# Kernel optimization log

Measured on AMD Instinct MI355X. Metric: run time of the kernel, lower is better.

## Reference

```python
import jax, jax.numpy as jnp
import numpy as np


def l2_normalize(x, axis, eps=1e-12):
    # matches tf.nn.l2_normalize / K.l2_normalize
    return x * jax.lax.rsqrt(jnp.maximum(jnp.sum(x * x, axis=axis, keepdims=True), eps))


def setup_inputs() -> dict:
    key = jax.random.key(0)
    k1, k2 = jax.random.split(key)
    B, H, W, C = 32, 1, 900, 256
    return {
        "input_1": jax.random.normal(k1, (B, H, W, C), dtype=jnp.float32),
        "input_2": jax.random.normal(k2, (B, H, W, C), dtype=jnp.float32),
    }


def reference(input_1, input_2):
    B, H, W, C = input_1.shape
    p = W // 2
    # 'euclidean' normalization along the width (azimuth) axis, axis=2
    x1 = l2_normalize(input_1, axis=2)
    x2 = l2_normalize(input_2, axis=2)
    # RangePadding2D: circular padding along width to width 2W-1, so that a
    # VALID correlation with a W-wide kernel yields exactly W circular shifts.
    x1p = jnp.concatenate([x1[:, :, p:, :], x1, x1[:, :, : p - 1, :]], axis=2)  # [B,H,2W-1,C]
    # Per-sample correlation: out[b, j] = sum_{h,i,c} x1p[b,h,j+i,c] * x2[b,h,i,c]
    # Expressed as one grouped conv (one group per batch element) instead of tf.scan.
    lhs = jnp.transpose(x1p, (0, 3, 1, 2)).reshape(1, B * C, H, 2 * W - 1)  # NCHW
    rhs = jnp.transpose(x2, (0, 3, 1, 2))  # [B, C, H, W] OIHW
    out = jax.lax.conv_general_dilated(
        lhs, rhs,
        window_strides=(1, 1), padding="VALID",
        dimension_numbers=("NCHW", "OIHW", "NCHW"),
        feature_group_count=B,
    )  # [1, B, 1, W]
    # -> (B, H=1, W, output_dim=1), matching compute_output_shape
    return jnp.transpose(out, (1, 2, 3, 0))
```

## Files before the change

kernel.cpp:

```cpp
#include <hip/hip_runtime.h>
#include <hip/hip_bf16.h>

#define BATCH 32
#define WW 900
#define CCH 256
#define PVAL 450
#define KHALF 128
#define MSTRIP 128
#define NCHUNK 64
#define NCHUNKS 15

typedef __bf16 bf16x8 __attribute__((ext_vector_type(8)));
typedef __bf16 bf16x4 __attribute__((ext_vector_type(4)));
typedef float f32x4 __attribute__((ext_vector_type(4)));

#define INV15_OFF 245760
#define INV4_OFF  65536

__global__ void nc_norm_partial(const float* __restrict__ x1,
                                const float* __restrict__ x2,
                                float* __restrict__ sums,
                                float* __restrict__ out, int out_n,
                                int segs, int rowsper) {
    int blk = blockIdx.x;
    int oz = blk * 256 + threadIdx.x;
    if (oz < out_n) out[oz] = 0.f;
    int seg = blk % segs;
    int b = (blk / segs) & 31;
    int which = blk / (segs * 32);
    const float* x = which ? x2 : x1;
    int c = threadIdx.x;
    int r0 = seg * rowsper;
    int r1 = r0 + rowsper;
    if (r1 > WW) r1 = WW;
    const float* p = x + ((size_t)b * WW + r0) * CCH + c;
    float s = 0.f;
    #pragma unroll 4
    for (int w = 0; w < r1 - r0; ++w) {
        float v = p[(size_t)w * CCH];
        s = fmaf(v, v, s);
    }
    sums[(((size_t)(which * 32 + b)) * segs + seg) * CCH + c] = s;
}

template <int SEGS>
__global__ void nc_norm_finalize(float* __restrict__ ws, float* __restrict__ inv) {
    int i = blockIdx.x * 256 + threadIdx.x;
    int c = i & 255;
    int wb = i >> 8;
    const float* s = ws + (size_t)wb * SEGS * CCH + c;
    float t = 0.f;
    #pragma unroll
    for (int q = 0; q < SEGS; ++q) t += s[(size_t)q * CCH];
    inv[i] = rsqrtf(fmaxf(t, 1e-12f));
}

__global__ __launch_bounds__(256, 2)
void nc_corr(const float* __restrict__ x1,
             const float* __restrict__ x2,
             const float* __restrict__ invp,
             float* __restrict__ out) {
    __shared__ __bf16 Abuf[MSTRIP * KHALF];
    __shared__ __bf16 Bbuf[2][NCHUNK * KHALF];
    __shared__ float diag[2][4][96];
    __shared__ float partial[WW];

    float (*scratch)[16][97] = (float (*)[16][97])Abuf;

    const int tid = threadIdx.x;
    const int b = blockIdx.x & 31;
    const int strip = (blockIdx.x >> 5) & 7;
    const int kh = blockIdx.x >> 8;
    const int m0 = strip * MSTRIP;
    const int k0 = kh * KHALF;

    const float* __restrict__ inv1 = invp + b * CCH + k0;
    const float* __restrict__ inv2 = invp + (BATCH + b) * CCH + k0;
    const float* __restrict__ x1b = x1 + (size_t)b * WW * CCH + k0;
    const float* __restrict__ x2b = x2 + (size_t)b * WW * CCH + k0;

    const int lane = tid & 63;
    const int wave = tid >> 6;
    const int fr = lane & 15;
    const int fq = lane >> 4;

    const int sr = tid >> 5;
    const int sg = tid & 31;

    const float4 ivB = *(const float4*)(inv2 + sg * 4);
    float4 st[8];

    auto loadB = [&](int chunk) {
        #pragma unroll
        for (int k = 0; k < 8; ++k) {
            const int row = chunk * NCHUNK + sr + 8 * k;
            st[k] = (row < WW) ? *(const float4*)(x2b + (size_t)row * CCH + sg * 4)
                               : make_float4(0.f, 0.f, 0.f, 0.f);
        }
    };
    auto writeB = [&](int buf) {
        #pragma unroll
        for (int k = 0; k < 8; ++k) {
            const int row = sr + 8 * k;
            float4 f = st[k];
            bf16x4 v = { (__bf16)(f.x * ivB.x), (__bf16)(f.y * ivB.y),
                         (__bf16)(f.z * ivB.z), (__bf16)(f.w * ivB.w) };
            *(bf16x4*)(&Bbuf[buf][row * KHALF + (((sg >> 1) ^ sr) << 3) + (sg & 1) * 4]) = v;
        }
    };

    loadB(0);

    {
        float4 iv1 = *(const float4*)(inv1 + sg * 4);
        #pragma unroll
        for (int k = 0; k < 16; ++k) {
            const int row = sr + 8 * k;
            const int m = m0 + row;
            float4 f = make_float4(0.f, 0.f, 0.f, 0.f);
            if (m < WW) f = *(const float4*)(x1b + (size_t)m * CCH + sg * 4);
            bf16x4 v = { (__bf16)(f.x * iv1.x), (__bf16)(f.y * iv1.y),
                         (__bf16)(f.z * iv1.z), (__bf16)(f.w * iv1.w) };
            *(bf16x4*)(&Abuf[row * KHALF + (((sg >> 1) ^ (row & 7)) << 3) + (sg & 1) * 4]) = v;
        }
    }

    for (int i = tid; i < WW; i += 256) partial[i] = 0.f;
    writeB(0);
    __syncthreads();

    bf16x8 afm[2][4];
    #pragma unroll
    for (int mt = 0; mt < 2; ++mt)
        #pragma unroll
        for (int kk = 0; kk < 4; ++kk) {
            const int row = wave * 32 + mt * 16 + fr;
            const int g = (kk * 4 + fq) ^ (row & 7);
            afm[mt][kk] = *(const bf16x8*)(&Abuf[row * KHALF + g * 8]);
        }
    #pragma unroll
    for (int mt = 0; mt < 2; ++mt)
        #pragma unroll
        for (int kk = 0; kk < 4; ++kk)
            asm volatile("" : "+v"(afm[mt][kk]));

    __syncthreads();

    {
        float* sw = (float*)&scratch[wave][0][0];
        for (int i = lane; i < 16 * 97; i += 64) sw[i] = 0.f;
    }

    int cur = 0;
    for (int chunk = 0; chunk < NCHUNKS; ++chunk) {
        if (chunk + 1 < NCHUNKS) {
            loadB(chunk + 1);
            __builtin_amdgcn_sched_barrier(0);
        }

        f32x4 acc[2][4];
        #pragma unroll
        for (int mt = 0; mt < 2; ++mt)
            #pragma unroll
            for (int nt = 0; nt < 4; ++nt)
                acc[mt][nt] = (f32x4){0.f, 0.f, 0.f, 0.f};

        #pragma unroll
        for (int kk = 0; kk < 4; ++kk) {
            bf16x8 bfr[4];
            #pragma unroll
            for (int nt = 0; nt < 4; ++nt) {
                const int row = nt * 16 + fr;
                const int g = (kk * 4 + fq) ^ (row & 7);
                bfr[nt] = *(const bf16x8*)(&Bbuf[cur][row * KHALF + g * 8]);
            }
            #pragma unroll
            for (int mt = 0; mt < 2; ++mt)
                #pragma unroll
                for (int nt = 0; nt < 4; ++nt)
                    acc[mt][nt] = __builtin_amdgcn_mfma_f32_16x16x32_bf16(
                        afm[mt][kk], bfr[nt], acc[mt][nt], 0, 0, 0);
        }

        {
            f32x4 c0 = acc[0][3];
            f32x4 c1 = acc[0][2] + acc[1][3];
            f32x4 c2 = acc[0][1] + acc[1][2];
            f32x4 c3 = acc[0][0] + acc[1][1];
            f32x4 c4 = acc[1][0];
            const int mub = 4 * fq;
            #pragma unroll
            for (int r = 0; r < 4; ++r) {
                const int mu = mub + r;
                const int drb = mu - fr + 15;
                scratch[wave][mu][drb]      = c0[r];
                scratch[wave][mu][drb + 16] = c1[r];
                scratch[wave][mu][drb + 32] = c2[r];
                scratch[wave][mu][drb + 48] = c3[r];
                scratch[wave][mu][drb + 64] = c4[r];
            }
        }

        {
            float s = 0.f, s2 = 0.f;
            #pragma unroll
            for (int m = 0; m < 16; ++m) {
                s  += scratch[wave][m][lane];
                s2 += scratch[wave][m][64 + lane];
            }
            diag[chunk & 1][wave][lane] = s;
            if (lane < 31) diag[chunk & 1][wave][64 + lane] = s2;
        }

        if (chunk + 1 < NCHUNKS) writeB(cur ^ 1);
        __syncthreads();

        if (tid < 191) {
            float s = 0.f;
            #pragma unroll
            for (int w = 0; w < 4; ++w) {
                const int dr = tid - 32 * w;
                if (dr >= 0 && dr < 95) s += diag[chunk & 1][w][dr];
            }
            int v = m0 - 64 * chunk + tid + 1287;
            if (v >= 1800) v -= 900;
            if (v >= 900) v -= 900;
            partial[v] += s;
        }
        cur ^= 1;
    }

    __syncthreads();
    for (int i = tid; i < WW; i += 256)
        unsafeAtomicAdd(&out[(size_t)b * WW + i], partial[i]);
}

extern "C" void kernel_launch(void* const* d_in, const int* in_sizes, int n_in,
                              void* d_out, int out_size, void* d_ws, size_t ws_size,
                              hipStream_t stream) {
    const float* x1 = (const float*)d_in[0];
    const float* x2 = (const float*)d_in[1];
    float* out = (float*)d_out;
    float* ws = (float*)d_ws;

    const size_t need15 = (size_t)(INV15_OFF + 16384) * sizeof(float);
    if (ws_size >= need15) {
        const int segs = 15, rowsper = 60;
        nc_norm_partial<<<2 * 32 * segs, 256, 0, stream>>>(x1, x2, ws, out, out_size, segs, rowsper);
        nc_norm_finalize<15><<<64, 256, 0, stream>>>(ws, ws + INV15_OFF);
        nc_corr<<<512, 256, 0, stream>>>(x1, x2, ws + INV15_OFF, out);
    } else {
        const int segs = 4, rowsper = 225;
        nc_norm_partial<<<2 * 32 * segs, 256, 0, stream>>>(x1, x2, ws, out, out_size, segs, rowsper);
        nc_norm_finalize<4><<<64, 256, 0, stream>>>(ws, ws + INV4_OFF);
        nc_corr<<<512, 256, 0, stream>>>(x1, x2, ws + INV4_OFF, out);
    }
}
```

Before: 50.25 us.

## Double M-strip per block to halve B-operand reloads, 256 blocks

Each correlation block now covers a 256-row strip of x1 instead of 128, with each wave holding four M-tiles in registers. This halves the number of blocks, so each x2 chunk is loaded and converted half as often across the grid, and it halves the atomic adds to the output. In exchange, occupancy drops to one block per CU, only 256 blocks run on a large GPU, and the diagonal reduction processes 8 virtual waves per step.

```diff
diff --git a/kernel.cpp b/kernel.cpp
--- a/kernel.cpp
+++ b/kernel.cpp
@@ -4,9 +4,8 @@
 #define BATCH 32
 #define WW 900
 #define CCH 256
-#define PVAL 450
 #define KHALF 128
-#define MSTRIP 128
+#define MSTRIP 256
 #define NCHUNK 64
 #define NCHUNKS 15
 
@@ -55,22 +54,22 @@
     inv[i] = rsqrtf(fmaxf(t, 1e-12f));
 }
 
-__global__ __launch_bounds__(256, 2)
+__global__ __launch_bounds__(256, 1)
 void nc_corr(const float* __restrict__ x1,
              const float* __restrict__ x2,
              const float* __restrict__ invp,
              float* __restrict__ out) {
     __shared__ __bf16 Abuf[MSTRIP * KHALF];
     __shared__ __bf16 Bbuf[2][NCHUNK * KHALF];
-    __shared__ float diag[2][4][96];
+    __shared__ float diag[2][8][96];
     __shared__ float partial[WW];
 
     float (*scratch)[16][97] = (float (*)[16][97])Abuf;
 
     const int tid = threadIdx.x;
     const int b = blockIdx.x & 31;
-    const int strip = (blockIdx.x >> 5) & 7;
-    const int kh = blockIdx.x >> 8;
+    const int strip = (blockIdx.x >> 5) & 3;
+    const int kh = blockIdx.x >> 7;
     const int m0 = strip * MSTRIP;
     const int k0 = kh * KHALF;
 
@@ -114,7 +113,7 @@
     {
         float4 iv1 = *(const float4*)(inv1 + sg * 4);
         #pragma unroll
-        for (int k = 0; k < 16; ++k) {
+        for (int k = 0; k < 32; ++k) {
             const int row = sr + 8 * k;
             const int m = m0 + row;
             float4 f = make_float4(0.f, 0.f, 0.f, 0.f);
@@ -129,17 +128,17 @@
     writeB(0);
     __syncthreads();
 
-    bf16x8 afm[2][4];
+    bf16x8 afm[4][4];
     #pragma unroll
-    for (int mt = 0; mt < 2; ++mt)
+    for (int mt = 0; mt < 4; ++mt)
         #pragma unroll
         for (int kk = 0; kk < 4; ++kk) {
-            const int row = wave * 32 + mt * 16 + fr;
+            const int row = wave * 64 + mt * 16 + fr;
             const int g = (kk * 4 + fq) ^ (row & 7);
             afm[mt][kk] = *(const bf16x8*)(&Abuf[row * KHALF + g * 8]);
         }
     #pragma unroll
-    for (int mt = 0; mt < 2; ++mt)
+    for (int mt = 0; mt < 4; ++mt)
         #pragma unroll
         for (int kk = 0; kk < 4; ++kk)
             asm volatile("" : "+v"(afm[mt][kk]));
@@ -147,8 +146,8 @@
     __syncthreads();
 
     {
-        float* sw = (float*)&scratch[wave][0][0];
-        for (int i = lane; i < 16 * 97; i += 64) sw[i] = 0.f;
+        float* sw = (float*)&scratch[2 * wave][0][0];
+        for (int i = lane; i < 2 * 16 * 97; i += 64) sw[i] = 0.f;
     }
 
     int cur = 0;
@@ -158,9 +157,9 @@
             __builtin_amdgcn_sched_barrier(0);
         }
 
-        f32x4 acc[2][4];
-        #pragma unroll
-        for (int mt = 0; mt < 2; ++mt)
+        f32x4 acc[4][4];
+        #pragma unroll
+        for (int mt = 0; mt < 4; ++mt)
             #pragma unroll
             for (int nt = 0; nt < 4; ++nt)
                 acc[mt][nt] = (f32x4){0.f, 0.f, 0.f, 0.f};
@@ -175,57 +174,67 @@
                 bfr[nt] = *(const bf16x8*)(&Bbuf[cur][row * KHALF + g * 8]);
             }
             #pragma unroll
-            for (int mt = 0; mt < 2; ++mt)
+            for (int mt = 0; mt < 4; ++mt)
                 #pragma unroll
                 for (int nt = 0; nt < 4; ++nt)
                     acc[mt][nt] = __builtin_amdgcn_mfma_f32_16x16x32_bf16(
                         afm[mt][kk], bfr[nt], acc[mt][nt], 0, 0, 0);
         }
 
-        {
-            f32x4 c0 = acc[0][3];
-            f32x4 c1 = acc[0][2] + acc[1][3];
-            f32x4 c2 = acc[0][1] + acc[1][2];
-            f32x4 c3 = acc[0][0] + acc[1][1];
-            f32x4 c4 = acc[1][0];
-            const int mub = 4 * fq;
-            #pragma unroll
-            for (int r = 0; r < 4; ++r) {
-                const int mu = mub + r;
-                const int drb = mu - fr + 15;
-                scratch[wave][mu][drb]      = c0[r];
-                scratch[wave][mu][drb + 16] = c1[r];
-                scratch[wave][mu][drb + 32] = c2[r];
-                scratch[wave][mu][drb + 48] = c3[r];
-                scratch[wave][mu][drb + 64] = c4[r];
-            }
-        }
-
-        {
-            float s = 0.f, s2 = 0.f;
-            #pragma unroll
-            for (int m = 0; m < 16; ++m) {
-                s  += scratch[wave][m][lane];
-                s2 += scratch[wave][m][64 + lane];
-            }
-            diag[chunk & 1][wave][lane] = s;
-            if (lane < 31) diag[chunk & 1][wave][64 + lane] = s2;
+        #pragma unroll
+        for (int h = 0; h < 2; ++h) {
+            const int vw = 2 * wave + h;
+            {
+                f32x4 c0 = acc[2*h+0][3];
+                f32x4 c1 = acc[2*h+0][2] + acc[2*h+1][3];
+                f32x4 c2 = acc[2*h+0][1] + acc[2*h+1][2];
+                f32x4 c3 = acc[2*h+0][0] + acc[2*h+1][1];
+                f32x4 c4 = acc[2*h+1][0];
+                const int mub = 4 * fq;
+                #pragma unroll
+                for (int r = 0; r < 4; ++r) {
+                    const int mu = mub + r;
+                    const int drb = mu - fr + 15;
+                    scratch[vw][mu][drb]      = c0[r];
+                    scratch[vw][mu][drb + 16] = c1[r];
+                    scratch[vw][mu][drb + 32] = c2[r];
+                    scratch[vw][mu][drb + 48] = c3[r];
+                    scratch[vw][mu][drb + 64] = c4[r];
+                }
+            }
+            {
+                float s = 0.f, s2 = 0.f;
+                #pragma unroll
+                for (int m = 0; m < 16; ++m) {
+                    s  += scratch[vw][m][lane];
+                    s2 += scratch[vw][m][64 + lane];
+                }
+                diag[chunk & 1][vw][lane] = s;
+                if (lane < 31) diag[chunk & 1][vw][64 + lane] = s2;
+            }
         }
 
         if (chunk + 1 < NCHUNKS) writeB(cur ^ 1);
         __syncthreads();
 
-        if (tid < 191) {
-            float s = 0.f;
-            #pragma unroll
-            for (int w = 0; w < 4; ++w) {
-                const int dr = tid - 32 * w;
-                if (dr >= 0 && dr < 95) s += diag[chunk & 1][w][dr];
-            }
-            int v = m0 - 64 * chunk + tid + 1287;
-            if (v >= 1800) v -= 900;
-            if (v >= 900) v -= 900;
-            partial[v] += s;
+        {
+            const int par = chunk & 1;
+            #pragma unroll
+            for (int pass = 0; pass < 2; ++pass) {
+                const int t = tid + pass * 256;
+                if (pass == 0 || tid < 63) {
+                    float s = 0.f;
+                    #pragma unroll
+                    for (int w = 0; w < 8; ++w) {
+                        const int dr = t - 32 * w;
+                        if (dr >= 0 && dr < 95) s += diag[par][w][dr];
+                    }
+                    int v = m0 - 64 * chunk + t + 1287;
+                    if (v >= 1800) v -= 900;
+                    if (v >= 900) v -= 900;
+                    partial[v] += s;
+                }
+            }
         }
         cur ^= 1;
     }
@@ -248,11 +257,11 @@
         const int segs = 15, rowsper = 60;
         nc_norm_partial<<<2 * 32 * segs, 256, 0, stream>>>(x1, x2, ws, out, out_size, segs, rowsper);
         nc_norm_finalize<15><<<64, 256, 0, stream>>>(ws, ws + INV15_OFF);
-        nc_corr<<<512, 256, 0, stream>>>(x1, x2, ws + INV15_OFF, out);
+        nc_corr<<<256, 256, 0, stream>>>(x1, x2, ws + INV15_OFF, out);
     } else {
         const int segs = 4, rowsper = 225;
         nc_norm_partial<<<2 * 32 * segs, 256, 0, stream>>>(x1, x2, ws, out, out_size, segs, rowsper);
         nc_norm_finalize<4><<<64, 256, 0, stream>>>(ws, ws + INV4_OFF);
-        nc_corr<<<512, 256, 0, stream>>>(x1, x2, ws + INV4_OFF, out);
-    }
-}
+        nc_corr<<<256, 256, 0, stream>>>(x1, x2, ws + INV4_OFF, out);
+    }
+}
```

New measurement: 58.05 us (median of 2 runs). 15.5% more time.
